# Performance work log

Hardware: AMD Instinct MI355X
Metric: run time of the kernel (lower is better)

## Reference

```python
import jax, jax.numpy as jnp
import numpy as np

N = 500_000      # total rows (e.g. video frames)
S = 10_000       # number of segments (shots)
D_IN = 128
D_OUT = 128


def setup_inputs() -> dict:
    key = jax.random.key(0)
    k1, k2, k3 = jax.random.split(key, 3)
    inp = jax.random.normal(k1, (N, D_IN), dtype=jnp.float32)
    # contiguous non-overlapping segments covering [0, N): graph[j] = (start_j, end_j) inclusive
    rng = np.random.default_rng(0)
    cuts = np.sort(rng.choice(np.arange(1, N), size=S - 1, replace=False))
    starts = np.concatenate([[0], cuts]).astype(np.int64)
    ends = np.concatenate([cuts - 1, [N - 1]]).astype(np.int64)
    graph = jnp.asarray(np.stack([starts, ends], axis=1))  # [S, 2]
    # nn.Linear params (kaiming-uniform-ish scale is irrelevant for correctness baseline)
    W = jax.random.normal(k2, (D_OUT, D_IN), dtype=jnp.float32) * (1.0 / np.sqrt(D_IN))
    b = jax.random.normal(k3, (D_OUT,), dtype=jnp.float32) * 0.01
    return {"input": inp, "graph": graph, "W": W, "b": b}


def reference(input, graph, W, b):
    # One big GEMM for the projection (instead of per-segment Linear calls) ...
    y = input @ W.T + b                              # [N, D_OUT]
    n = input.shape[0]
    s = graph.shape[0]
    starts = graph[:, 0]
    ends = graph[:, 1]
    rows = jnp.arange(n)
    # ... then a single irregular segment reduction over ragged boundaries.
    seg_id = jnp.clip(jnp.searchsorted(starts, rows, side="right") - 1, 0, s - 1)  # [N]
    valid = (rows >= starts[seg_id]) & (rows <= ends[seg_id])  # guards any uncovered rows
    y = jnp.where(valid[:, None], y, 0.0)
    return jax.ops.segment_sum(y, seg_id, num_segments=s)     # [S, D_OUT]
```

## Files before the change

### kernel.cpp

```cpp
#include <hip/hip_runtime.h>
#include <hip/hip_bf16.h>


#define D 128
#define D4 32
#define CHUNK 256

__device__ __forceinline__ void f4add(float4& a, const float4& v) {
  a.x += v.x; a.y += v.y; a.z += v.z; a.w += v.w;
}

__global__ __launch_bounds__(256) void zero_xs_kernel(float4* Xs4, int n4) {
  int i = blockIdx.x * 256 + threadIdx.x;
  if (i < n4) Xs4[i] = make_float4(0.f, 0.f, 0.f, 0.f);
}

__global__ __launch_bounds__(256) void seg_sum_chunk_kernel(
    const float* __restrict__ in, const int* __restrict__ graph,
    float* __restrict__ Xs, int N, int S) {
  int tid = threadIdx.x;
  int c4  = tid & 31;
  int rg  = tid >> 5;

  int row0   = blockIdx.x * CHUNK;
  int rowEnd = min(row0 + CHUNK, N) - 1;
  if (row0 > rowEnd) return;

  int lo = 0, hi = S - 1;
  while (lo < hi) {
    int mid = (lo + hi + 1) >> 1;
    if (graph[2 * mid] <= row0) lo = mid; else hi = mid - 1;
  }

  __shared__ float4 buf[2][3][32];
  const float4* in4 = (const float4*)in;
  int parity = 0;

  int s = lo;
  while (true) {
    int rs    = graph[2 * s];
    int reRaw = graph[2 * s + 1];
    int nxt   = (s + 1 < S) ? graph[2 * s + 2] : N;
    int re    = min(reRaw, min(nxt - 1, N - 1));
    int rs_c  = max(rs, 0);
    int a     = max(rs_c, row0);
    int b2    = min(re, rowEnd);

    if (a <= b2) {
      int len = b2 - a + 1;
      const float4* p = in4 + (size_t)a * D4 + c4;
      float4 acc0 = make_float4(0.f, 0.f, 0.f, 0.f);
      float4 acc1 = make_float4(0.f, 0.f, 0.f, 0.f);
      int r = rg;
      for (; r + 8 < len; r += 16) {
        float4 v0 = p[(size_t)r * D4];
        float4 v1 = p[(size_t)(r + 8) * D4];
        f4add(acc0, v0);
        f4add(acc1, v1);
      }
      for (; r < len; r += 8) f4add(acc0, p[(size_t)r * D4]);
      f4add(acc0, acc1);

      float4 o;
      o.x = __shfl_xor(acc0.x, 32, 64);
      o.y = __shfl_xor(acc0.y, 32, 64);
      o.z = __shfl_xor(acc0.z, 32, 64);
      o.w = __shfl_xor(acc0.w, 32, 64);
      f4add(acc0, o);

      int wv = tid >> 6;
      if ((tid & 32) == 0 && wv > 0) buf[parity][wv - 1][c4] = acc0;
      __syncthreads();
      if (tid < 32) {
        f4add(acc0, buf[parity][0][c4]);
        f4add(acc0, buf[parity][1][c4]);
        f4add(acc0, buf[parity][2][c4]);
        bool full = (rs_c >= row0) && (re <= rowEnd);
        if (full) {
          ((float4*)Xs)[(size_t)s * D4 + c4] = acc0;
        } else {
          float* q = Xs + (size_t)s * D + c4 * 4;
          atomicAdd(q + 0, acc0.x);
          atomicAdd(q + 1, acc0.y);
          atomicAdd(q + 2, acc0.z);
          atomicAdd(q + 3, acc0.w);
        }
      }
      parity ^= 1;
    }
    if (s + 1 >= S || graph[2 * s + 2] > rowEnd) break;
    ++s;
  }
}

#define SEG_PB 16
#define OUT_PB 64
#define WT_STRIDE 65

__global__ __launch_bounds__(256) void seg_gemm_kernel(
    const float* __restrict__ Xs, const float* __restrict__ W,
    const float* __restrict__ b, const int* __restrict__ graph,
    float* __restrict__ out, int N, int S) {
  __shared__ float Wt[D * WT_STRIDE];
  __shared__ __align__(16) float XsL[SEG_PB * D];
  __shared__ float cntL[SEG_PB];

  int tid   = threadIdx.x;
  int s0    = blockIdx.x * SEG_PB;
  int oBase = blockIdx.y * OUT_PB;

  #pragma unroll
  for (int rnd = 0; rnd < 8; ++rnd) {
    int linear = rnd * 256 + tid;
    int op     = linear >> 5;
    int d4     = (linear & 31) << 2;
    float4 w = *(const float4*)(W + (oBase + op) * D + d4);
    Wt[(d4 + 0) * WT_STRIDE + op] = w.x;
    Wt[(d4 + 1) * WT_STRIDE + op] = w.y;
    Wt[(d4 + 2) * WT_STRIDE + op] = w.z;
    Wt[(d4 + 3) * WT_STRIDE + op] = w.w;
  }
  {
    const float4* src = (const float4*)(Xs + s0 * D);
    float4* dst = (float4*)XsL;
    dst[tid]       = src[tid];
    dst[tid + 256] = src[tid + 256];
  }
  if (tid < SEG_PB) {
    int s   = s0 + tid;
    int rs  = graph[2 * s];
    int re  = graph[2 * s + 1];
    int nxt = (s + 1 < S) ? (graph[2 * s + 2] - 1) : (N - 1);
    re = min(re, min(nxt, N - 1));
    rs = max(rs, 0);
    cntL[tid] = (float)max(0, re - rs + 1);
  }
  __syncthreads();

  int op = tid & 63;
  int g  = tid >> 6;
  float acc[4] = {0.f, 0.f, 0.f, 0.f};

  const float4* xs4 = (const float4*)XsL;
  #pragma unroll 8
  for (int d4 = 0; d4 < D4; ++d4) {
    float w0 = Wt[(4 * d4 + 0) * WT_STRIDE + op];
    float w1 = Wt[(4 * d4 + 1) * WT_STRIDE + op];
    float w2 = Wt[(4 * d4 + 2) * WT_STRIDE + op];
    float w3 = Wt[(4 * d4 + 3) * WT_STRIDE + op];
    #pragma unroll
    for (int j = 0; j < 4; ++j) {
      float4 x = xs4[(4 * j + g) * D4 + d4];
      acc[j] += x.x * w0 + x.y * w1 + x.z * w2 + x.w * w3;
    }
  }

  float bo = b[oBase + op];
  #pragma unroll
  for (int j = 0; j < 4; ++j) {
    int sl = 4 * j + g;
    out[(s0 + sl) * D + oBase + op] = acc[j] + cntL[sl] * bo;
  }
}

extern "C" void kernel_launch(void* const* d_in, const int* in_sizes, int n_in,
                              void* d_out, int out_size, void* d_ws, size_t ws_size,
                              hipStream_t stream) {
  const float* in    = (const float*)d_in[0];
  const int*   graph = (const int*)d_in[1];
  const float* W     = (const float*)d_in[2];
  const float* b     = (const float*)d_in[3];
  float* out = (float*)d_out;

  const int N = in_sizes[0] / D;
  const int S = in_sizes[1] / 2;

  float* Xs = (float*)d_ws;

  int n4 = S * D4;
  zero_xs_kernel<<<(n4 + 255) / 256, 256, 0, stream>>>((float4*)Xs, n4);

  int nBlocks = (N + CHUNK - 1) / CHUNK;
  seg_sum_chunk_kernel<<<nBlocks, 256, 0, stream>>>(in, graph, Xs, N, S);

  dim3 grid2(S / SEG_PB, D / OUT_PB);
  seg_gemm_kernel<<<grid2, 256, 0, stream>>>(Xs, W, b, graph, out, N, S);
}
```

Baseline: 377.0 us.

## Assign independent row windows per wavefront to remove block-level syncs

Replaces the 256-row block-cooperative segment reduction with per-wavefront 128-row windows. Each wave does its own binary search and segment walk, and combines across half-waves with a shuffle. This drops the shared-memory cross-wave reduction and the __syncthreads issued per segment. The inner loop also gets four independent accumulators for more memory-level parallelism. In exchange, segments that span window boundaries are split more often, which adds atomicAdd traffic and more binary searches.

```diff
diff --git a/kernel.cpp b/kernel.cpp
--- a/kernel.cpp
+++ b/kernel.cpp
@@ -4,7 +4,7 @@
 
 #define D 128
 #define D4 32
-#define CHUNK 256
+#define WROWS 128
 
 __device__ __forceinline__ void f4add(float4& a, const float4& v) {
   a.x += v.x; a.y += v.y; a.z += v.z; a.w += v.w;
@@ -15,80 +15,76 @@
   if (i < n4) Xs4[i] = make_float4(0.f, 0.f, 0.f, 0.f);
 }
 
-__global__ __launch_bounds__(256) void seg_sum_chunk_kernel(
+__global__ __launch_bounds__(256) void seg_sum_wave_kernel(
     const float* __restrict__ in, const int* __restrict__ graph,
     float* __restrict__ Xs, int N, int S) {
-  int tid = threadIdx.x;
-  int c4  = tid & 31;
-  int rg  = tid >> 5;
+  int lane = threadIdx.x & 63;
+  int wv   = threadIdx.x >> 6;
+  int win  = blockIdx.x * 4 + wv;
+  int w0   = win * WROWS;
+  if (w0 >= N) return;
+  int wEnd = min(w0 + WROWS, N) - 1;
 
-  int row0   = blockIdx.x * CHUNK;
-  int rowEnd = min(row0 + CHUNK, N) - 1;
-  if (row0 > rowEnd) return;
+  int c4 = lane & 31;
+  int rh = lane >> 5;
 
   int lo = 0, hi = S - 1;
   while (lo < hi) {
     int mid = (lo + hi + 1) >> 1;
-    if (graph[2 * mid] <= row0) lo = mid; else hi = mid - 1;
+    if (graph[2 * mid] <= w0) lo = mid; else hi = mid - 1;
   }
 
-  __shared__ float4 buf[2][3][32];
   const float4* in4 = (const float4*)in;
-  int parity = 0;
-
   int s = lo;
   while (true) {
-    int rs    = graph[2 * s];
-    int reRaw = graph[2 * s + 1];
-    int nxt   = (s + 1 < S) ? graph[2 * s + 2] : N;
-    int re    = min(reRaw, min(nxt - 1, N - 1));
-    int rs_c  = max(rs, 0);
-    int a     = max(rs_c, row0);
-    int b2    = min(re, rowEnd);
+    int rs       = graph[2 * s];
+    int reRaw    = graph[2 * s + 1];
+    int nxtStart = (s + 1 < S) ? graph[2 * s + 2] : N;
+    int re       = min(reRaw, min(nxtStart - 1, N - 1));
+    int rs_c     = max(rs, 0);
+    int a        = max(rs_c, w0);
+    int b2       = min(re, wEnd);
 
     if (a <= b2) {
       int len = b2 - a + 1;
-      const float4* p = in4 + (size_t)a * D4 + c4;
-      float4 acc0 = make_float4(0.f, 0.f, 0.f, 0.f);
-      float4 acc1 = make_float4(0.f, 0.f, 0.f, 0.f);
-      int r = rg;
-      for (; r + 8 < len; r += 16) {
-        float4 v0 = p[(size_t)r * D4];
-        float4 v1 = p[(size_t)(r + 8) * D4];
-        f4add(acc0, v0);
-        f4add(acc1, v1);
+      const float4* p = in4 + (size_t)(a + rh) * D4 + c4;
+      float4 A0 = make_float4(0.f,0.f,0.f,0.f);
+      float4 A1 = make_float4(0.f,0.f,0.f,0.f);
+      float4 A2 = make_float4(0.f,0.f,0.f,0.f);
+      float4 A3 = make_float4(0.f,0.f,0.f,0.f);
+      int r = 0;
+      for (; r + 8 <= len; r += 8) {
+        float4 v0 = p[(size_t)(r + 0) * D4];
+        float4 v1 = p[(size_t)(r + 2) * D4];
+        float4 v2 = p[(size_t)(r + 4) * D4];
+        float4 v3 = p[(size_t)(r + 6) * D4];
+        f4add(A0, v0); f4add(A1, v1); f4add(A2, v2); f4add(A3, v3);
       }
-      for (; r < len; r += 8) f4add(acc0, p[(size_t)r * D4]);
-      f4add(acc0, acc1);
+      for (; r + rh < len; r += 2)
+        f4add(A0, p[(size_t)r * D4]);
+      f4add(A0, A1); f4add(A2, A3); f4add(A0, A2);
 
       float4 o;
-      o.x = __shfl_xor(acc0.x, 32, 64);
-      o.y = __shfl_xor(acc0.y, 32, 64);
-      o.z = __shfl_xor(acc0.z, 32, 64);
-      o.w = __shfl_xor(acc0.w, 32, 64);
-      f4add(acc0, o);
+      o.x = __shfl_xor(A0.x, 32, 64);
+      o.y = __shfl_xor(A0.y, 32, 64);
+      o.z = __shfl_xor(A0.z, 32, 64);
+      o.w = __shfl_xor(A0.w, 32, 64);
+      f4add(A0, o);
 
-      int wv = tid >> 6;
-      if ((tid & 32) == 0 && wv > 0) buf[parity][wv - 1][c4] = acc0;
-      __syncthreads();
-      if (tid < 32) {
-        f4add(acc0, buf[parity][0][c4]);
-        f4add(acc0, buf[parity][1][c4]);
-        f4add(acc0, buf[parity][2][c4]);
-        bool full = (rs_c >= row0) && (re <= rowEnd);
+      bool full = (rs_c >= w0) && (re <= wEnd);
+      if (lane < 32) {
         if (full) {
-          ((float4*)Xs)[(size_t)s * D4 + c4] = acc0;
+          ((float4*)Xs)[(size_t)s * D4 + c4] = A0;
         } else {
           float* q = Xs + (size_t)s * D + c4 * 4;
-          atomicAdd(q + 0, acc0.x);
-          atomicAdd(q + 1, acc0.y);
-          atomicAdd(q + 2, acc0.z);
-          atomicAdd(q + 3, acc0.w);
+          atomicAdd(q + 0, A0.x);
+          atomicAdd(q + 1, A0.y);
+          atomicAdd(q + 2, A0.z);
+          atomicAdd(q + 3, A0.w);
         }
       }
-      parity ^= 1;
     }
-    if (s + 1 >= S || graph[2 * s + 2] > rowEnd) break;
+    if (s + 1 >= S || graph[2 * s + 2] > wEnd) break;
     ++s;
   }
 }
@@ -180,8 +176,9 @@
   int n4 = S * D4;
   zero_xs_kernel<<<(n4 + 255) / 256, 256, 0, stream>>>((float4*)Xs, n4);
 
-  int nBlocks = (N + CHUNK - 1) / CHUNK;
-  seg_sum_chunk_kernel<<<nBlocks, 256, 0, stream>>>(in, graph, Xs, N, S);
+  int nWaves  = (N + WROWS - 1) / WROWS;
+  int nBlocks = (nWaves + 3) / 4;
+  seg_sum_wave_kernel<<<nBlocks, 256, 0, stream>>>(in, graph, Xs, N, S);
 
   dim3 grid2(S / SEG_PB, D / OUT_PB);
   seg_gemm_kernel<<<grid2, 256, 0, stream>>>(Xs, W, b, graph, out, N, S);
```

Result: no change. 381.5 us (+1.2%).
